# Optimization experiments

Measured on AMD Instinct MI355X. Metric: run time of the kernel, lower is better.

Reference implementation:

```python
import jax, jax.numpy as jnp
import numpy as np
import math

EMBED_DIM = 1024
NUM_HEADS = 16
HEAD_DIM = EMBED_DIM // NUM_HEADS
BATCH = 2
SEQ = 2048


def setup_inputs() -> dict:
    key = jax.random.key(0)
    ks = jax.random.split(key, 9)
    s = 1.0 / math.sqrt(EMBED_DIM)
    return {
        "x": jax.random.normal(ks[0], (BATCH, SEQ, EMBED_DIM), jnp.float32),
        "Wq": jax.random.normal(ks[1], (EMBED_DIM, EMBED_DIM), jnp.float32) * s,
        "bq": jnp.zeros((EMBED_DIM,), jnp.float32),
        "Wk": jax.random.normal(ks[2], (EMBED_DIM, EMBED_DIM), jnp.float32) * s,
        "bk": jnp.zeros((EMBED_DIM,), jnp.float32),
        "Wv": jax.random.normal(ks[3], (EMBED_DIM, EMBED_DIM), jnp.float32) * s,
        "bv": jnp.zeros((EMBED_DIM,), jnp.float32),
        "Wo": jax.random.normal(ks[4], (EMBED_DIM, EMBED_DIM), jnp.float32) * s,
        "bo": jnp.zeros((EMBED_DIM,), jnp.float32),
    }


def _rope_tables(seq_len, dim, dtype):
    inv_freq = 1.0 / (10000.0 ** (jnp.arange(0, dim, 2, dtype=jnp.float32) / dim))
    t = jnp.arange(seq_len, dtype=jnp.float32)
    freqs = jnp.einsum("i,j->ij", t, inv_freq)          # [S, D/2]
    emb = jnp.concatenate([freqs, freqs], axis=-1)       # [S, D]
    return jnp.cos(emb).astype(dtype), jnp.sin(emb).astype(dtype)


def _rotate_half(x):
    x1, x2 = jnp.split(x, 2, axis=-1)
    return jnp.concatenate([-x2, x1], axis=-1)


def _apply_rope(x, cos, sin):
    # x: [B, S, H, D]; cos/sin: [S, D] -> broadcast over batch & heads
    cos = cos[None, :, None, :]
    sin = sin[None, :, None, :]
    return x * cos + _rotate_half(x) * sin


def reference(x, Wq, bq, Wk, bk, Wv, bv, Wo, bo):
    B, S, E = x.shape
    H, D = NUM_HEADS, HEAD_DIM
    q = (x @ Wq + bq).reshape(B, S, H, D)
    k = (x @ Wk + bk).reshape(B, S, H, D)
    v = (x @ Wv + bv).reshape(B, S, H, D)
    cos, sin = _rope_tables(S, D, x.dtype)
    q = _apply_rope(q, cos, sin)
    k = _apply_rope(k, cos, sin)
    scale = 1.0 / math.sqrt(D)
    # scores: [B, H, S, S]
    scores = jnp.einsum("bqhd,bkhd->bhqk", q, k) * scale
    attn = jax.nn.softmax(scores, axis=-1)
    ctx = jnp.einsum("bhqk,bkhd->bqhd", attn, v).reshape(B, S, E)
    return ctx @ Wo + bo
```

## Files before the change

kernel.cpp:

```cpp
#include <hip/hip_runtime.h>
#include <math.h>

#define B_ 2
#define S_ 2048
#define E_ 1024
#define H_ 16
#define D_ 64
#define M_ (B_*S_)

typedef _Float16 f16x8  __attribute__((ext_vector_type(8)));
typedef _Float16 f16x4v __attribute__((ext_vector_type(4)));
typedef __fp16   h16x2  __attribute__((ext_vector_type(2)));
typedef float    f32x4  __attribute__((ext_vector_type(4)));

__device__ __forceinline__ ushort f2h(float f) {
    _Float16 h = (_Float16)f;
    return __builtin_bit_cast(ushort, h);
}

__device__ __forceinline__ void gload_lds16(const ushort* g, ushort* l) {
    __builtin_amdgcn_global_load_lds(
        (const __attribute__((address_space(1))) unsigned int*)g,
        (__attribute__((address_space(3))) unsigned int*)l, 16, 0, 0);
}

__global__ void prep_kernel(const float* __restrict__ x,
                            const float* __restrict__ W0, const float* __restrict__ W1,
                            const float* __restrict__ W2, const float* __restrict__ W3,
                            ushort* __restrict__ xf, ushort* __restrict__ WT,
                            float* __restrict__ ct, float* __restrict__ st)
{
    const int bid = blockIdx.x;
    const int tid = threadIdx.x;
    __shared__ float tile[32][33];

    if (bid < 4096) {
        const int z = bid >> 10, rem = bid & 1023;
        const int k0 = (rem >> 5) * 32, nb = (rem & 31) * 32;
        const float* W = (z == 0) ? W0 : (z == 1) ? W1 : (z == 2) ? W2 : W3;
        const size_t zoff = (size_t)z * E_ * E_;
        const int tx = tid & 31, ty = tid >> 5;
        #pragma unroll
        for (int i = 0; i < 4; i++) {
            int r = i * 8 + ty;
            tile[r][tx] = W[(size_t)(k0 + r) * E_ + nb + tx];
        }
        __syncthreads();
        #pragma unroll
        for (int i = 0; i < 4; i++) {
            int r = i * 8 + ty;
            WT[zoff + (size_t)(nb + r) * E_ + k0 + tx] = f2h(tile[tx][r]);
        }
    } else if (bid < 8192) {
        const int i = (bid - 4096) * 1024 + tid * 4;
        float4 v = *(const float4*)&x[i];
        *(ushort4*)&xf[i] = make_ushort4(f2h(v.x), f2h(v.y), f2h(v.z), f2h(v.w));
    } else {
        const int i = (bid - 8192) * 256 + tid;
        const int j = i & 31, pos = i >> 5;
        float invf = (float)pow(10000.0, -(double)j / 32.0);
        float ang  = (float)pos * invf;
        ct[i] = (float)cos((double)ang);
        st[i] = (float)sin((double)ang);
    }
}

#define GBM 128
#define GBN 128
#define GBK 32

__global__ __launch_bounds__(256, 3)
void gemm_f16(const ushort* __restrict__ A, const ushort* __restrict__ WTp,
              const float* __restrict__ b0, const float* __restrict__ b1,
              const float* __restrict__ b2,
              const float* __restrict__ ct, const float* __restrict__ st,
              ushort* __restrict__ outQ, ushort* __restrict__ outK,
              ushort* __restrict__ outV, float* __restrict__ outF,
              int force_mode)
{
    __shared__ __align__(16) ushort lA[2][GBM * GBK];
    __shared__ __align__(16) ushort lB[2][GBN * GBK];

    const int tid  = threadIdx.x;
    const int wv   = tid >> 6, lane = tid & 63;
    const int c    = lane & 15, qd = lane >> 4;
    const int rh   = wv >> 1, chn = wv & 1;

    int mode, nx;
    size_t zoff;
    if (force_mode >= 0) { mode = force_mode; nx = blockIdx.x; zoff = 0; }
    else { mode = blockIdx.x >> 3; nx = blockIdx.x & 7; zoff = (size_t)mode * (E_ * E_); }
    const ushort* Bt = WTp + zoff;

    const int m0 = blockIdx.y * GBM, n0 = nx * GBN;

    const ushort* gsrc = (wv < 2) ? A : Bt;
    const int rowbase = ((wv < 2) ? m0 : n0) + (wv & 1) * 64;
    const int lofs = (wv & 1) * 64 * GBK;
    const int srow = lane >> 2;
    const int soct = (lane & 3) * 8;

    f32x4 acc[4][4] = {};

    #pragma unroll
    for (int cc = 0; cc < 4; cc++) {
        const ushort* g = gsrc + (size_t)(rowbase + cc * 16 + srow) * E_ + soct;
        gload_lds16(g, ((wv < 2) ? &lA[0][0] : &lB[0][0]) + lofs + cc * 512);
    }
    __syncthreads();

    for (int t = 0; t < E_ / GBK; t++) {
        if (t < E_ / GBK - 1) {
            const int nb = (t + 1) & 1;
            const int k0i = (t + 1) * GBK;
            ushort* dst = ((wv < 2) ? &lA[nb][0] : &lB[nb][0]) + lofs;
            #pragma unroll
            for (int cc = 0; cc < 4; cc++) {
                const ushort* g = gsrc + (size_t)(rowbase + cc * 16 + srow) * E_ + k0i + soct;
                gload_lds16(g, dst + cc * 512);
            }
        }

        const ushort* Ab = lA[t & 1];
        const ushort* Bb = lB[t & 1];

        f16x8 af[4], bf[4];
        #pragma unroll
        for (int mt = 0; mt < 4; mt++)
            af[mt] = *(const f16x8*)&Ab[(rh * 64 + mt * 16 + c) * GBK + qd * 8];
        #pragma unroll
        for (int nt = 0; nt < 4; nt++)
            bf[nt] = *(const f16x8*)&Bb[(chn * 64 + nt * 16 + c) * GBK + qd * 8];
        #pragma unroll
        for (int mt = 0; mt < 4; mt++)
            #pragma unroll
            for (int nt = 0; nt < 4; nt++)
                acc[mt][nt] = __builtin_amdgcn_mfma_f32_16x16x32_f16(af[mt], bf[nt], acc[mt][nt], 0, 0, 0);
        __syncthreads();
    }

    const float* bias = (mode == 0) ? b0 : (mode == 1) ? b1 : (mode == 2) ? b2 : b0;
    const int colbase = n0 + chn * 64;

    if (mode == 3) {
        #pragma unroll
        for (int mt = 0; mt < 4; mt++)
            #pragma unroll
            for (int r = 0; r < 4; r++) {
                const int row = m0 + rh * 64 + mt * 16 + qd * 4 + r;
                #pragma unroll
                for (int nt = 0; nt < 4; nt++) {
                    const int col = colbase + nt * 16 + c;
                    outF[(size_t)row * E_ + col] = acc[mt][nt][r] + bias[col];
                }
            }
    } else if (mode == 2) {
        const int hd = colbase >> 6;
        #pragma unroll
        for (int mt = 0; mt < 4; mt++)
            #pragma unroll
            for (int r = 0; r < 4; r++) {
                const int row = m0 + rh * 64 + mt * 16 + qd * 4 + r;
                const int bb = row >> 11, sl = row & (S_ - 1);
                const int tt = sl >> 7, key = sl & 127;
                const int c4 = key >> 2, inner = key & 3;
                const size_t base = (size_t)(bb * H_ + hd) * (S_ * D_) + tt * 8192;
                #pragma unroll
                for (int nt = 0; nt < 4; nt++) {
                    const int d = nt * 16 + c;
                    outV[base + d * 128 + ((c4 ^ (d & 7)) * 4) + inner]
                        = f2h(acc[mt][nt][r] + bias[colbase + d]);
                }
            }
    } else {
        ushort* O = (mode == 0) ? outQ : outK;
        const float sc = (mode == 0) ? 0.125f : 1.0f;
        #pragma unroll
        for (int mt = 0; mt < 4; mt++)
            #pragma unroll
            for (int r = 0; r < 4; r++) {
                const int row = m0 + rh * 64 + mt * 16 + qd * 4 + r;
                const int pos = row & (S_ - 1);
                const int sw = row & 7;
                #pragma unroll
                for (int p = 0; p < 2; p++) {
                    const int j32 = p * 16 + c;
                    const float cth = ct[pos * 32 + j32], sth = st[pos * 32 + j32];
                    const float v1 = acc[mt][p][r]     + bias[colbase + p * 16 + c];
                    const float v2 = acc[mt][p + 2][r] + bias[colbase + (p + 2) * 16 + c];
                    const float o1 = (v1 * cth - v2 * sth) * sc;
                    const float o2 = (v2 * cth + v1 * sth) * sc;
                    const int cd1 = p * 16 + c, cd2 = cd1 + 32;
                    O[(size_t)row * E_ + colbase + (((cd1 >> 3) ^ sw) * 8) + (cd1 & 7)] = f2h(o1);
                    O[(size_t)row * E_ + colbase + (((cd2 >> 3) ^ sw) * 8) + (cd2 & 7)] = f2h(o2);
                }
            }
    }
}

__global__ __launch_bounds__(256, 2)
void attn_mfma(const ushort* __restrict__ Qf, const ushort* __restrict__ Kf,
               const ushort* __restrict__ Vfg, ushort* __restrict__ ctxf)
{
    __shared__ __align__(16) ushort Kls[2][128 * 64];
    __shared__ __align__(16) ushort Vls[2][64 * 128];

    const int tid = threadIdx.x;
    const int wv = tid >> 6, lane = tid & 63;
    const int c = lane & 15, qd = lane >> 4;
    const int cs = c & 7;

    const int xcd = blockIdx.x & 7, ii = blockIdx.x >> 3;
    const int bh = xcd * 4 + (ii & 3);
    const int qtb = ii >> 2;
    const int b = bh >> 4, h = bh & 15;
    const int q0 = qtb * 64;

    const size_t qrow0 = (size_t)b * S_ + q0;
    const size_t krow0 = (size_t)b * S_;
    const size_t vbase = (size_t)bh * (S_ * D_);

    const int l8 = lane >> 3, l7 = lane & 7;
    const int l16 = lane >> 4, l15 = lane & 15;

    #pragma unroll
    for (int j = 0; j < 2; j++) {
        const int row = wv * 16 + j * 8 + l8;
        const ushort* g = Qf + (qrow0 + row) * E_ + h * 64 + l7 * 8;
        gload_lds16(g, &Kls[0][wv * 1024 + j * 512]);
    }
    __syncthreads();
    f16x8 qfrag[4][2];
    #pragma unroll
    for (int qt = 0; qt < 4; qt++)
        #pragma unroll
        for (int kc = 0; kc < 2; kc++)
            qfrag[qt][kc] = *(const f16x8*)&Kls[0][(qt * 16 + c) * 64 + (((kc * 4 + qd) ^ cs) * 8)];
    __syncthreads();

    f32x4 acc[4][4] = {};
    float lsum[4] = {0.f, 0.f, 0.f, 0.f};

    if (wv < 2) {
        #pragma unroll
        for (int j = 0; j < 8; j++) {
            const int row = wv * 64 + j * 8 + l8;
            gload_lds16(Kf + (krow0 + row) * E_ + h * 64 + l7 * 8,
                        &Kls[0][wv * 4096 + j * 512]);
        }
    } else {
        #pragma unroll
        for (int j = 0; j < 8; j++) {
            const int drow = (wv - 2) * 32 + j * 4 + l16;
            gload_lds16(Vfg + vbase + drow * 128 + l15 * 8,
                        &Vls[0][(wv - 2) * 4096 + j * 512]);
        }
    }
    __syncthreads();

    #pragma unroll 1
    for (int t = 0; t < 16; t++) {
        if (t < 15) {
            const int nb = (t + 1) & 1;
            const int k0n = (t + 1) * 128;
            if (wv < 2) {
                #pragma unroll
                for (int j = 0; j < 8; j++) {
                    const int row = wv * 64 + j * 8 + l8;
                    gload_lds16(Kf + (krow0 + k0n + row) * E_ + h * 64 + l7 * 8,
                                &Kls[nb][wv * 4096 + j * 512]);
                }
            } else {
                #pragma unroll
                for (int j = 0; j < 8; j++) {
                    const int drow = (wv - 2) * 32 + j * 4 + l16;
                    gload_lds16(Vfg + vbase + (t + 1) * 8192 + drow * 128 + l15 * 8,
                                &Vls[nb][(wv - 2) * 4096 + j * 512]);
                }
            }
        }

        const ushort* kb = Kls[t & 1];
        const ushort* vb = Vls[t & 1];

        f16x4v bfrag[2][4];
        #pragma unroll
        for (int kt = 0; kt < 2; kt++) {
            f16x8 kfr[2];
            #pragma unroll
            for (int kc = 0; kc < 2; kc++)
                kfr[kc] = *(const f16x8*)&kb[(wv * 32 + kt * 16 + c) * 64 + (((kc * 4 + qd) ^ cs) * 8)];
            #pragma unroll
            for (int qt = 0; qt < 4; qt++) {
                f32x4 s = {};
                s = __builtin_amdgcn_mfma_f32_16x16x32_f16(kfr[0], qfrag[qt][0], s, 0, 0, 0);
                s = __builtin_amdgcn_mfma_f32_16x16x32_f16(kfr[1], qfrag[qt][1], s, 0, 0, 0);
                const float p0 = __expf(s[0]), p1 = __expf(s[1]);
                const float p2 = __expf(s[2]), p3 = __expf(s[3]);
                lsum[qt] += (p0 + p1) + (p2 + p3);
                h16x2 lo = __builtin_amdgcn_cvt_pkrtz(p0, p1);
                h16x2 hi = __builtin_amdgcn_cvt_pkrtz(p2, p3);
                uint2 u;
                u.x = __builtin_bit_cast(unsigned int, lo);
                u.y = __builtin_bit_cast(unsigned int, hi);
                bfrag[kt][qt] = __builtin_bit_cast(f16x4v, u);
            }
        }

        #pragma unroll
        for (int dt = 0; dt < 4; dt++) {
            #pragma unroll
            for (int kt = 0; kt < 2; kt++) {
                f16x4v vfr = *(const f16x4v*)&vb[(dt * 16 + c) * 128 + (((wv * 8 + kt * 4 + qd) ^ cs) * 4)];
                #pragma unroll
                for (int qt = 0; qt < 4; qt++)
                    acc[dt][qt] = __builtin_amdgcn_mfma_f32_16x16x16f16(vfr, bfrag[kt][qt], acc[dt][qt], 0, 0, 0);
            }
        }
        __syncthreads();
    }

    float* red = (float*)&Kls[0][0];
    float* lsr = (float*)&Vls[0][0];

    #pragma unroll
    for (int qt = 0; qt < 4; qt++) {
        float v = lsum[qt];
        v += __shfl_xor(v, 16);
        v += __shfl_xor(v, 32);
        lsum[qt] = v;
    }
    if (lane < 16) {
        #pragma unroll
        for (int qt = 0; qt < 4; qt++) lsr[wv * 64 + qt * 16 + lane] = lsum[qt];
    }

    f32x4 own[4];
    #pragma unroll
    for (int qt = 0; qt < 4; qt++)
        own[qt] = (wv == 0) ? acc[0][qt] : (wv == 1) ? acc[1][qt]
                : (wv == 2) ? acc[2][qt] : acc[3][qt];

    #pragma unroll
    for (int r = 1; r < 4; r++) {
        const int ds = (wv + r) & 3;
        #pragma unroll
        for (int qt = 0; qt < 4; qt++) {
            f32x4 sv = (ds == 0) ? acc[0][qt] : (ds == 1) ? acc[1][qt]
                     : (ds == 2) ? acc[2][qt] : acc[3][qt];
            *(f32x4*)&red[ds * 1024 + qt * 256 + lane * 4] = sv;
        }
        __syncthreads();
        #pragma unroll
        for (int qt = 0; qt < 4; qt++)
            own[qt] += *(const f32x4*)&red[wv * 1024 + qt * 256 + lane * 4];
        if (r < 3) __syncthreads();
    }

    float inv[4];
    #pragma unroll
    for (int qt = 0; qt < 4; qt++) {
        const int q = qt * 16 + c;
        inv[qt] = 1.0f / (lsr[q] + lsr[64 + q] + lsr[128 + q] + lsr[192 + q]);
    }

    const size_t obase = qrow0 * E_ + h * 64 + wv * 16 + qd * 4;
    #pragma unroll
    for (int qt = 0; qt < 4; qt++) {
        f32x4 v = own[qt];
        const float iq = inv[qt];
        ushort4 o = make_ushort4(f2h(v[0] * iq), f2h(v[1] * iq),
                                 f2h(v[2] * iq), f2h(v[3] * iq));
        *(ushort4*)&ctxf[obase + (size_t)(qt * 16 + c) * E_] = o;
    }
}

extern "C" void kernel_launch(void* const* d_in, const int* in_sizes, int n_in,
                              void* d_out, int out_size, void* d_ws, size_t ws_size,
                              hipStream_t stream)
{
    const float* x  = (const float*)d_in[0];
    const float* Wq = (const float*)d_in[1];
    const float* bq = (const float*)d_in[2];
    const float* Wk = (const float*)d_in[3];
    const float* bk = (const float*)d_in[4];
    const float* Wv = (const float*)d_in[5];
    const float* bv = (const float*)d_in[6];
    const float* Wo = (const float*)d_in[7];
    const float* bo = (const float*)d_in[8];
    float* out = (float*)d_out;

    ushort* Qb = (ushort*)d_ws;
    ushort* Kb = Qb + (size_t)M_ * E_;
    ushort* Vf = Kb + (size_t)M_ * E_;
    ushort* xf = Vf + (size_t)M_ * E_;
    ushort* WT = xf + (size_t)M_ * E_;
    float*  ct = (float*)(WT + (size_t)4 * E_ * E_);
    float*  st = ct + S_ * 32;
    ushort* ctxf = Qb;

    hipLaunchKernelGGL(prep_kernel, dim3(8448), dim3(256), 0, stream,
                       x, Wq, Wk, Wv, Wo, xf, WT, ct, st);

    hipLaunchKernelGGL(gemm_f16, dim3(24, 32), dim3(256), 0, stream,
                       xf, WT, bq, bk, bv, ct, st,
                       Qb, Kb, Vf, (float*)nullptr, -1);

    hipLaunchKernelGGL(attn_mfma, dim3(B_ * H_ * (S_ / 64)), dim3(256), 0, stream,
                       Qb, Kb, Vf, ctxf);

    hipLaunchKernelGGL(gemm_f16, dim3(E_ / GBN, M_ / GBM), dim3(256), 0, stream,
                       ctxf, WT + (size_t)3 * E_ * E_, bo, bo, bo, ct, st,
                       (ushort*)nullptr, (ushort*)nullptr, (ushort*)nullptr, out, 3);
}
```

Measured before the change: 206.5 us.

## Halve attention key tile, raise occupancy, and use exp2 with log2e-scaled Q

The attention kernel now streams 64-key K/V tiles instead of 128. This halves LDS per block and raises launch bounds to 4 blocks per CU, to improve latency hiding, at the cost of twice as many loop iterations and barriers. The V tile loads pick one half of each stored 128-key swizzled block. Softmax uses the hardware exp2 with log2(e) folded into the Q scaling in the projection GEMM epilogue. The QKV GEMM grid also moves the projection index to blockIdx.z, which changes block ordering.

```diff
diff --git a/kernel.cpp b/kernel.cpp
--- a/kernel.cpp
+++ b/kernel.cpp
@@ -22,6 +22,10 @@
     __builtin_amdgcn_global_load_lds(
         (const __attribute__((address_space(1))) unsigned int*)g,
         (__attribute__((address_space(3))) unsigned int*)l, 16, 0, 0);
+}
+
+__device__ __forceinline__ float exp2_fast(float x) {
+    return __builtin_amdgcn_exp2f(x);
 }
 
 __global__ void prep_kernel(const float* __restrict__ x,
@@ -68,6 +72,7 @@
 #define GBM 128
 #define GBN 128
 #define GBK 32
+#define LOG2E 1.44269504088896340736f
 
 __global__ __launch_bounds__(256, 3)
 void gemm_f16(const ushort* __restrict__ A, const ushort* __restrict__ WTp,
@@ -86,13 +91,11 @@
     const int c    = lane & 15, qd = lane >> 4;
     const int rh   = wv >> 1, chn = wv & 1;
 
-    int mode, nx;
-    size_t zoff;
-    if (force_mode >= 0) { mode = force_mode; nx = blockIdx.x; zoff = 0; }
-    else { mode = blockIdx.x >> 3; nx = blockIdx.x & 7; zoff = (size_t)mode * (E_ * E_); }
+    const int mode = (force_mode >= 0) ? force_mode : (int)blockIdx.z;
+    const size_t zoff = (force_mode >= 0) ? 0 : (size_t)blockIdx.z * (E_ * E_);
     const ushort* Bt = WTp + zoff;
 
-    const int m0 = blockIdx.y * GBM, n0 = nx * GBN;
+    const int m0 = blockIdx.y * GBM, n0 = blockIdx.x * GBN;
 
     const ushort* gsrc = (wv < 2) ? A : Bt;
     const int rowbase = ((wv < 2) ? m0 : n0) + (wv & 1) * 64;
@@ -174,7 +177,7 @@
             }
     } else {
         ushort* O = (mode == 0) ? outQ : outK;
-        const float sc = (mode == 0) ? 0.125f : 1.0f;
+        const float sc = (mode == 0) ? 0.125f * LOG2E : 1.0f;
         #pragma unroll
         for (int mt = 0; mt < 4; mt++)
             #pragma unroll
@@ -198,12 +201,12 @@
     }
 }
 
-__global__ __launch_bounds__(256, 2)
+__global__ __launch_bounds__(256, 4)
 void attn_mfma(const ushort* __restrict__ Qf, const ushort* __restrict__ Kf,
                const ushort* __restrict__ Vfg, ushort* __restrict__ ctxf)
 {
-    __shared__ __align__(16) ushort Kls[2][128 * 64];
-    __shared__ __align__(16) ushort Vls[2][64 * 128];
+    __shared__ __align__(16) ushort Kls[2][64 * 64];
+    __shared__ __align__(16) ushort Vls[2][64 * 64];
 
     const int tid = threadIdx.x;
     const int wv = tid >> 6, lane = tid & 63;
@@ -221,13 +224,12 @@
     const size_t vbase = (size_t)bh * (S_ * D_);
 
     const int l8 = lane >> 3, l7 = lane & 7;
-    const int l16 = lane >> 4, l15 = lane & 15;
 
     #pragma unroll
     for (int j = 0; j < 2; j++) {
         const int row = wv * 16 + j * 8 + l8;
-        const ushort* g = Qf + (qrow0 + row) * E_ + h * 64 + l7 * 8;
-        gload_lds16(g, &Kls[0][wv * 1024 + j * 512]);
+        gload_lds16(Qf + (qrow0 + row) * E_ + h * 64 + l7 * 8,
+                    &Kls[0][wv * 1024 + j * 512]);
     }
     __syncthreads();
     f16x8 qfrag[4][2];
@@ -243,39 +245,40 @@
 
     if (wv < 2) {
         #pragma unroll
-        for (int j = 0; j < 8; j++) {
-            const int row = wv * 64 + j * 8 + l8;
+        for (int j = 0; j < 4; j++) {
+            const int row = wv * 32 + j * 8 + l8;
             gload_lds16(Kf + (krow0 + row) * E_ + h * 64 + l7 * 8,
-                        &Kls[0][wv * 4096 + j * 512]);
+                        &Kls[0][wv * 2048 + j * 512]);
         }
     } else {
         #pragma unroll
-        for (int j = 0; j < 8; j++) {
-            const int drow = (wv - 2) * 32 + j * 4 + l16;
-            gload_lds16(Vfg + vbase + drow * 128 + l15 * 8,
-                        &Vls[0][(wv - 2) * 4096 + j * 512]);
+        for (int j = 0; j < 4; j++) {
+            const int drow = (wv - 2) * 32 + j * 8 + l8;
+            gload_lds16(Vfg + vbase + drow * 128 + l7 * 8,
+                        &Vls[0][(wv - 2) * 2048 + j * 512]);
         }
     }
     __syncthreads();
 
     #pragma unroll 1
-    for (int t = 0; t < 16; t++) {
-        if (t < 15) {
+    for (int t = 0; t < 32; t++) {
+        if (t < 31) {
             const int nb = (t + 1) & 1;
-            const int k0n = (t + 1) * 128;
+            const int k0n = (t + 1) * 64;
+            const int tt = (t + 1) >> 1, half = (t + 1) & 1;
             if (wv < 2) {
                 #pragma unroll
-                for (int j = 0; j < 8; j++) {
-                    const int row = wv * 64 + j * 8 + l8;
+                for (int j = 0; j < 4; j++) {
+                    const int row = wv * 32 + j * 8 + l8;
                     gload_lds16(Kf + (krow0 + k0n + row) * E_ + h * 64 + l7 * 8,
-                                &Kls[nb][wv * 4096 + j * 512]);
+                                &Kls[nb][wv * 2048 + j * 512]);
                 }
             } else {
                 #pragma unroll
-                for (int j = 0; j < 8; j++) {
-                    const int drow = (wv - 2) * 32 + j * 4 + l16;
-                    gload_lds16(Vfg + vbase + (t + 1) * 8192 + drow * 128 + l15 * 8,
-                                &Vls[nb][(wv - 2) * 4096 + j * 512]);
+                for (int j = 0; j < 4; j++) {
+                    const int drow = (wv - 2) * 32 + j * 8 + l8;
+                    gload_lds16(Vfg + vbase + tt * 8192 + drow * 128 + half * 64 + l7 * 8,
+                                &Vls[nb][(wv - 2) * 2048 + j * 512]);
                 }
             }
         }
@@ -283,39 +286,34 @@
         const ushort* kb = Kls[t & 1];
         const ushort* vb = Vls[t & 1];
 
-        f16x4v bfrag[2][4];
-        #pragma unroll
-        for (int kt = 0; kt < 2; kt++) {
-            f16x8 kfr[2];
-            #pragma unroll
-            for (int kc = 0; kc < 2; kc++)
-                kfr[kc] = *(const f16x8*)&kb[(wv * 32 + kt * 16 + c) * 64 + (((kc * 4 + qd) ^ cs) * 8)];
-            #pragma unroll
-            for (int qt = 0; qt < 4; qt++) {
-                f32x4 s = {};
-                s = __builtin_amdgcn_mfma_f32_16x16x32_f16(kfr[0], qfrag[qt][0], s, 0, 0, 0);
-                s = __builtin_amdgcn_mfma_f32_16x16x32_f16(kfr[1], qfrag[qt][1], s, 0, 0, 0);
-                const float p0 = __expf(s[0]), p1 = __expf(s[1]);
-                const float p2 = __expf(s[2]), p3 = __expf(s[3]);
-                lsum[qt] += (p0 + p1) + (p2 + p3);
-                h16x2 lo = __builtin_amdgcn_cvt_pkrtz(p0, p1);
-                h16x2 hi = __builtin_amdgcn_cvt_pkrtz(p2, p3);
-                uint2 u;
-                u.x = __builtin_bit_cast(unsigned int, lo);
-                u.y = __builtin_bit_cast(unsigned int, hi);
-                bfrag[kt][qt] = __builtin_bit_cast(f16x4v, u);
-            }
+        f16x8 kfr[2];
+        #pragma unroll
+        for (int kc = 0; kc < 2; kc++)
+            kfr[kc] = *(const f16x8*)&kb[(wv * 16 + c) * 64 + (((kc * 4 + qd) ^ cs) * 8)];
+
+        f16x4v bfrag[4];
+        #pragma unroll
+        for (int qt = 0; qt < 4; qt++) {
+            f32x4 s = {};
+            s = __builtin_amdgcn_mfma_f32_16x16x32_f16(kfr[0], qfrag[qt][0], s, 0, 0, 0);
+            s = __builtin_amdgcn_mfma_f32_16x16x32_f16(kfr[1], qfrag[qt][1], s, 0, 0, 0);
+            const float p0 = exp2_fast(s[0]), p1 = exp2_fast(s[1]);
+            const float p2 = exp2_fast(s[2]), p3 = exp2_fast(s[3]);
+            lsum[qt] += (p0 + p1) + (p2 + p3);
+            h16x2 lo = __builtin_amdgcn_cvt_pkrtz(p0, p1);
+            h16x2 hi = __builtin_amdgcn_cvt_pkrtz(p2, p3);
+            uint2 u;
+            u.x = __builtin_bit_cast(unsigned int, lo);
+            u.y = __builtin_bit_cast(unsigned int, hi);
+            bfrag[qt] = __builtin_bit_cast(f16x4v, u);
         }
 
         #pragma unroll
         for (int dt = 0; dt < 4; dt++) {
-            #pragma unroll
-            for (int kt = 0; kt < 2; kt++) {
-                f16x4v vfr = *(const f16x4v*)&vb[(dt * 16 + c) * 128 + (((wv * 8 + kt * 4 + qd) ^ cs) * 4)];
-                #pragma unroll
-                for (int qt = 0; qt < 4; qt++)
-                    acc[dt][qt] = __builtin_amdgcn_mfma_f32_16x16x16f16(vfr, bfrag[kt][qt], acc[dt][qt], 0, 0, 0);
-            }
+            f16x4v vfr = *(const f16x4v*)&vb[(dt * 16 + c) * 64 + (((wv * 4 + qd) ^ cs) * 4)];
+            #pragma unroll
+            for (int qt = 0; qt < 4; qt++)
+                acc[dt][qt] = __builtin_amdgcn_mfma_f32_16x16x16f16(vfr, bfrag[qt], acc[dt][qt], 0, 0, 0);
         }
         __syncthreads();
     }
@@ -402,7 +400,7 @@
     hipLaunchKernelGGL(prep_kernel, dim3(8448), dim3(256), 0, stream,
                        x, Wq, Wk, Wv, Wo, xf, WT, ct, st);
 
-    hipLaunchKernelGGL(gemm_f16, dim3(24, 32), dim3(256), 0, stream,
+    hipLaunchKernelGGL(gemm_f16, dim3(E_ / GBN, M_ / GBM, 3), dim3(256), 0, stream,
                        xf, WT, bq, bk, bv, ct, st,
                        Qb, Kb, Vf, (float*)nullptr, -1);
 
```

After: 227.7 us. 10.3% more time.
